# Kernel tuning notes

Hardware: AMD Instinct MI355X
Metric: run time of the kernel (lower is better)

The kernel has to match this reference:

```python
import jax, jax.numpy as jnp
import numpy as np

B, S, C, NH = 4, 2048, 1024, 16
HD = C // NH


def setup_inputs() -> dict:
    key = jax.random.key(0)
    ks = jax.random.split(key, 8)
    w = lambda k, shape: (jax.random.normal(k, shape, dtype=jnp.float32) * 0.02)
    return {
        "x": jax.random.normal(ks[0], (B, S, C), dtype=jnp.float32),
        "y": jax.random.normal(ks[1], (B, S, C), dtype=jnp.float32),
        "mask": jnp.zeros((B, S), dtype=bool),  # True = padded key
        "Wq_w": w(ks[2], (C, C)),
        "Wq_b": jnp.zeros((C,), dtype=jnp.float32),
        "Wkv_w": w(ks[3], (2 * C, C)),
        "Wkv_b": jnp.zeros((2 * C,), dtype=jnp.float32),
        "Wo_w": w(ks[4], (C, C)),
        "Wo_b": jnp.zeros((C,), dtype=jnp.float32),
    }


def reference(x, y, mask, Wq_w, Wq_b, Wkv_w, Wkv_b, Wo_w, Wo_b):
    b, s, c = x.shape
    # projections (torch nn.Linear: x @ W.T + b)
    q = (x @ Wq_w.T + Wq_b).reshape(b, s, NH, HD).transpose(0, 2, 1, 3)  # bhsd
    kv = (y @ Wkv_w.T + Wkv_b).reshape(b, s, 2, NH, HD)
    k = kv[:, :, 0].transpose(0, 2, 1, 3)  # bhsd
    v = kv[:, :, 1].transpose(0, 2, 1, 3)  # bhsd
    # scores: [b, h, s_q, s_k]
    attn = jnp.einsum("bhqd,bhkd->bhqk", q, k) / np.sqrt(HD).astype(np.float32)
    causal = jnp.triu(jnp.ones((s, s), dtype=bool), 1)  # True above diagonal
    combined = causal[None, None] | mask[:, None, None, :]
    attn = jnp.where(combined, -jnp.inf, attn)
    attn = jax.nn.softmax(attn, axis=-1)
    out = jnp.einsum("bhqk,bhkd->bhqd", attn, v)
    out = out.transpose(0, 2, 1, 3).reshape(b, s, c)
    return out @ Wo_w.T + Wo_b
```

## Files before the change

kernel.cpp:

```cpp
#include <hip/hip_runtime.h>
#include <stdint.h>

#define B_  4
#define S_  2048
#define C_  1024
#define NH_ 16
#define HD_ 64
#define M_  (B_*S_)
#define NT_ (S_/64)
#define NKT 16

typedef __attribute__((ext_vector_type(8))) short bf16x8;
typedef __attribute__((ext_vector_type(4))) float f32x4;

typedef __attribute__((address_space(1))) const unsigned int gu32;
typedef __attribute__((address_space(3))) unsigned int lu32;

__device__ __forceinline__ void gload16(const void* g, void* l) {
    __builtin_amdgcn_global_load_lds((gu32*)g, (lu32*)l, 16, 0, 0);
}

__device__ __forceinline__ unsigned short f2bf(float f) {
    union { float f; unsigned u; } v; v.f = f;
    unsigned r = v.u + 0x7FFF + ((v.u >> 16) & 1);
    return (unsigned short)(r >> 16);
}

__global__ __launch_bounds__(256)
void cvt_all(const float4* __restrict__ x, const float4* __restrict__ y,
             const float4* __restrict__ wq, const float4* __restrict__ wkv,
             const float4* __restrict__ wo,
             uint4* __restrict__ xb, uint4* __restrict__ yb, uint4* __restrict__ wqb,
             uint4* __restrict__ wkvb, uint4* __restrict__ wob) {
    int i = blockIdx.x * 256 + threadIdx.x;
    const float4* src; uint4* dst; int off;
    if      (i < 1048576) { src = x;   dst = xb;   off = i; }
    else if (i < 2097152) { src = y;   dst = yb;   off = i - 1048576; }
    else if (i < 2228224) { src = wq;  dst = wqb;  off = i - 2097152; }
    else if (i < 2490368) { src = wkv; dst = wkvb; off = i - 2228224; }
    else                  { src = wo;  dst = wob;  off = i - 2490368; }
    float4 a = src[2*off], b = src[2*off+1];
    union { unsigned short s[8]; uint4 v; } u;
    u.s[0]=f2bf(a.x); u.s[1]=f2bf(a.y); u.s[2]=f2bf(a.z); u.s[3]=f2bf(a.w);
    u.s[4]=f2bf(b.x); u.s[5]=f2bf(b.y); u.s[6]=f2bf(b.z); u.s[7]=f2bf(b.w);
    dst[off] = u.v;
}


#define STAGE_A(mi, kb, db) do { \
    gload16(gA + (size_t)(mi)*64*1024 + (kb),           sh + (db)*32768 + (w*8 + (mi)*64)*64); \
    gload16(gA + ((size_t)(mi)*64 + 128)*1024 + (kb),   sh + (db)*32768 + (w*8 + 128 + (mi)*64)*64); \
} while (0)

#define STAGE_B(ni, kb, db) do { \
    gload16(gB + (size_t)(ni)*32*1024 + (kb),           sh + (db)*32768 + 16384 + ((w>>2)*64 + (w&3)*8 + (ni)*32)*64); \
    gload16(gB + ((size_t)(ni)*32 + 128)*1024 + (kb),   sh + (db)*32768 + 16384 + ((w>>2)*64 + (w&3)*8 + (ni)*32 + 128)*64); \
} while (0)

#define READ_A(half) do { \
    _Pragma("unroll") \
    for (int mf = 0; mf < 4; ++mf) { \
        int idx = (wy*128 + (half)*64 + mf*16 + l16)*64 + colb; \
        af[mf][0] = *(const bf16x8*)&Asb[idx]; \
        af[mf][1] = *(const bf16x8*)&Asb[idx ^ 32]; \
    } \
} while (0)

#define READ_B(half) do { \
    _Pragma("unroll") \
    for (int nf = 0; nf < 2; ++nf) { \
        int idx = (wx*64 + (half)*32 + nf*16 + l16)*64 + colb; \
        bfv[half][nf][0] = *(const bf16x8*)&Bsb[idx]; \
        bfv[half][nf][1] = *(const bf16x8*)&Bsb[idx ^ 32]; \
    } \
} while (0)

#define MFMA_Q(mi, ni) do { \
    _Pragma("unroll") \
    for (int mf = 0; mf < 4; ++mf) { \
        _Pragma("unroll") \
        for (int nf = 0; nf < 2; ++nf) { \
            acc[mi][ni][mf][nf] = __builtin_amdgcn_mfma_f32_16x16x32_bf16(af[mf][0], bfv[ni][nf][0], acc[mi][ni][mf][nf], 0, 0, 0); \
            acc[mi][ni][mf][nf] = __builtin_amdgcn_mfma_f32_16x16x32_bf16(af[mf][1], bfv[ni][nf][1], acc[mi][ni][mf][nf], 0, 0, 0); \
        } \
    } \
} while (0)

template<int MODE>
__device__ __forceinline__
void gemm256_body(const unsigned short* __restrict__ A, const unsigned short* __restrict__ Bt,
                  const float* __restrict__ bias,
                  unsigned short* __restrict__ out0, unsigned short* __restrict__ out1,
                  float* __restrict__ outf, int bx, int by, unsigned short* sh)
{
    const int t = threadIdx.x;
    const int lane = t & 63, w = t >> 6;
    const int quad = lane >> 4, l16 = lane & 15;
    const int wy = w >> 2, wx = w & 3;
    const int s7 = l16 & 7;
    const int colb = (quad ^ s7) << 3;
    const int c16 = (lane & 7) ^ (lane >> 3);

    const int rowA0 = by * 256;
    const int colB0 = bx * 256;

    const unsigned short* gA = A  + (size_t)(rowA0 + w*8 + (lane>>3))*1024 + c16*8;
    const unsigned short* gB = Bt + (size_t)(colB0 + (w>>2)*64 + (w&3)*8 + (lane>>3))*1024 + c16*8;

    f32x4 acc[2][2][4][2] = {};
    bf16x8 af[4][2], bfv[2][2][2];

    STAGE_A(0, 0, 0);
    STAGE_B(1, 0, 0);
    STAGE_B(0, 0, 0);
    STAGE_A(1, 0, 0);
    STAGE_A(0, 64, 1);
    STAGE_B(1, 64, 1);
    asm volatile("s_waitcnt vmcnt(6)" ::: "memory");
    __builtin_amdgcn_s_barrier();
    __builtin_amdgcn_sched_barrier(0);

    #pragma unroll 1
    for (int kt = 0; kt < NKT; ++kt) {
        const int cur = kt & 1;
        const unsigned short* Asb = sh + cur*32768;
        const unsigned short* Bsb = Asb + 16384;
        const int kb1 = (kt + 1) * 64;
        const int kb2 = (kt + 2) * 64;
        const bool st1 = (kt + 1 < NKT);
        const bool st2 = (kt + 2 < NKT);

        if (st1) STAGE_B(0, kb1, cur ^ 1);
        READ_A(0);
        READ_B(0);
        __builtin_amdgcn_s_setprio(1);
        MFMA_Q(0, 0);
        __builtin_amdgcn_s_setprio(0);

        if (st1) STAGE_A(1, kb1, cur ^ 1);
        READ_B(1);
        __builtin_amdgcn_s_setprio(1);
        MFMA_Q(0, 1);
        __builtin_amdgcn_s_setprio(0);
        if (st1) asm volatile("s_waitcnt vmcnt(8)" ::: "memory");
        else     asm volatile("s_waitcnt vmcnt(0)" ::: "memory");
        __builtin_amdgcn_s_barrier();
        __builtin_amdgcn_sched_barrier(0);

        if (st2) STAGE_A(0, kb2, cur);
        READ_A(1);
        __builtin_amdgcn_s_setprio(1);
        MFMA_Q(1, 1);
        __builtin_amdgcn_s_setprio(0);

        if (st2) STAGE_B(1, kb2, cur);
        __builtin_amdgcn_s_setprio(1);
        MFMA_Q(1, 0);
        __builtin_amdgcn_s_setprio(0);
        if      (st2) asm volatile("s_waitcnt vmcnt(6)" ::: "memory");
        else if (st1) asm volatile("s_waitcnt vmcnt(2)" ::: "memory");
        __builtin_amdgcn_s_barrier();
        __builtin_amdgcn_sched_barrier(0);
    }

    const float QSCALE = 0.180336880111f;
    #pragma unroll
    for (int mi = 0; mi < 2; ++mi)
    #pragma unroll
    for (int ni = 0; ni < 2; ++ni)
    #pragma unroll
    for (int nf = 0; nf < 2; ++nf) {
        int gn = colB0 + wx*64 + ni*32 + nf*16 + l16;
        float bv = bias[gn];
        #pragma unroll
        for (int mf = 0; mf < 4; ++mf) {
            #pragma unroll
            for (int r = 0; r < 4; ++r) {
                int gm = rowA0 + wy*128 + mi*64 + mf*16 + quad*4 + r;
                float v = acc[mi][ni][mf][nf][r] + bv;
                if (MODE == 2) {
                    outf[(size_t)gm * 1024 + gn] = v;
                } else if (MODE == 0) {
                    v *= QSCALE;
                    int b = gm >> 11, s = gm & 2047;
                    int h = gn >> 6,  d = gn & 63;
                    out0[(((size_t)(b*NH_ + h)*S_ + s) << 6) + d] = f2bf(v);
                } else {
                    int b = gm >> 11, s = gm & 2047;
                    if (gn < C_) {
                        int h = gn >> 6, d = gn & 63;
                        out0[(((size_t)(b*NH_ + h)*S_ + s) << 6) + d] = f2bf(v);
                    } else {
                        int n2 = gn - C_;
                        int h = n2 >> 6, d = n2 & 63;
                        out1[((size_t)(b*NH_ + h)*HD_ + d)*S_ + s] = f2bf(v);
                    }
                }
            }
        }
    }
}

__global__ __launch_bounds__(512, 2)
void proj_fused256(const unsigned short* __restrict__ xb, const unsigned short* __restrict__ Wqb,
                   const float* __restrict__ Wq_b,
                   const unsigned short* __restrict__ yb, const unsigned short* __restrict__ Wkvb,
                   const float* __restrict__ Wkv_b,
                   unsigned short* __restrict__ Qg, unsigned short* __restrict__ Kg,
                   unsigned short* __restrict__ Vt)
{
    extern __shared__ unsigned short sh[];
    int bid = blockIdx.x;
    int id = (bid & 7) * 48 + (bid >> 3);
    if (id < 128) {
        gemm256_body<0>(xb, Wqb, Wq_b, Qg, nullptr, nullptr, id & 3, id >> 2, sh);
    } else {
        int j = id - 128;
        gemm256_body<1>(yb, Wkvb, Wkv_b, Kg, Vt, nullptr, j & 7, j >> 3, sh);
    }
}

__global__ __launch_bounds__(512, 2)
void gemm_oproj256(const unsigned short* __restrict__ A, const unsigned short* __restrict__ Bt,
                   const float* __restrict__ bias, float* __restrict__ outf)
{
    extern __shared__ unsigned short sh[];
    int id = ((blockIdx.x & 7) << 4) + (blockIdx.x >> 3);
    gemm256_body<2>(A, Bt, bias, nullptr, nullptr, outf, id & 3, id >> 2, sh);
}

__global__ __launch_bounds__(256, 4)
void attn_kernel(const unsigned short* __restrict__ Qg, const unsigned short* __restrict__ Kg,
                 const unsigned short* __restrict__ Vt, const unsigned char* __restrict__ maskp,
                 unsigned short* __restrict__ att)
{
    __shared__ unsigned short Pl[64*72];
    __shared__ float Lbuf[4][64];
    __shared__ float Linv[64];
    int t = threadIdx.x, lane = t & 63, w = t >> 6;
    int quad = lane >> 4, l16 = lane & 15;
    int bh = blockIdx.x, b = bh >> 4, h = bh & 15;
    int qi = blockIdx.y;

    const unsigned short* kbase = Kg + ((size_t)bh*S_ + w*16 + l16)*HD_ + quad*8;
    const unsigned short* vbase = Vt + ((size_t)bh*HD_ + w*16 + l16)*S_ + quad*8;
    int kp_row = w*16 + quad*4;
    const unsigned char* mbase = maskp + (size_t)b*S_ + kp_row;

    for (int half = 0; half < 2; ++half) {
        int qt = half ? (NT_ - 1 - qi) : qi;

        bf16x8 qf[4][2];
        #pragma unroll
        for (int m = 0; m < 4; ++m) {
            const unsigned short* qp = Qg + ((size_t)bh*S_ + qt*64 + m*16 + l16)*HD_;
            qf[m][0] = *reinterpret_cast<const bf16x8*>(qp + quad*8);
            qf[m][1] = *reinterpret_cast<const bf16x8*>(qp + 32 + quad*8);
        }
        f32x4 oacc[4] = {};
        float lsum[4] = {0.f, 0.f, 0.f, 0.f};

        bf16x8 kc0 = *reinterpret_cast<const bf16x8*>(kbase);
        bf16x8 kc1 = *reinterpret_cast<const bf16x8*>(kbase + 32);

        for (int kt = 0; kt <= qt; ++kt) {
            int ktn = (kt < qt) ? kt + 1 : kt;
            const unsigned short* kpn = kbase + (size_t)ktn*64*HD_;
            bf16x8 kn0 = *reinterpret_cast<const bf16x8*>(kpn);
            bf16x8 kn1 = *reinterpret_cast<const bf16x8*>(kpn + 32);
            const unsigned short* vp = vbase + kt*64;
            bf16x8 vc0 = *reinterpret_cast<const bf16x8*>(vp);
            bf16x8 vc1 = *reinterpret_cast<const bf16x8*>(vp + 32);

            unsigned m4 = *reinterpret_cast<const unsigned*>(mbase + kt*64);

            f32x4 sacc[4];
            #pragma unroll
            for (int m = 0; m < 4; ++m) {
                sacc[m] = __builtin_amdgcn_mfma_f32_16x16x32_bf16(kc0, qf[m][0], f32x4{}, 0, 0, 0);
                sacc[m] = __builtin_amdgcn_mfma_f32_16x16x32_bf16(kc1, qf[m][1], sacc[m], 0, 0, 0);
            }

            bool diag = (kt == qt);
            #pragma unroll
            for (int m = 0; m < 4; ++m) {
                float p[4];
                if (diag) {
                    #pragma unroll
                    for (int r = 0; r < 4; ++r) {
                        float s = sacc[m][r];
                        if (kp_row + r > m*16 + l16) s = -1e30f;
                        p[r] = __builtin_amdgcn_exp2f(s);
                    }
                } else {
                    #pragma unroll
                    for (int r = 0; r < 4; ++r)
                        p[r] = __builtin_amdgcn_exp2f(sacc[m][r]);
                }
                if (m4) {
                    #pragma unroll
                    for (int r = 0; r < 4; ++r)
                        if ((m4 >> (8*r)) & 0xFFu) p[r] = 0.f;
                }
                lsum[m] += (p[0] + p[1]) + (p[2] + p[3]);
                unsigned a01 = __builtin_amdgcn_perm(__float_as_uint(p[1]), __float_as_uint(p[0]), 0x07060302u);
                unsigned a23 = __builtin_amdgcn_perm(__float_as_uint(p[3]), __float_as_uint(p[2]), 0x07060302u);
                *reinterpret_cast<uint2*>(&Pl[(m*16 + l16)*72 + w*16 + quad*4]) = make_uint2(a01, a23);
            }
            __syncthreads();
            #pragma unroll
            for (int m = 0; m < 4; ++m) {
                bf16x8 pf0 = *reinterpret_cast<const bf16x8*>(&Pl[(m*16 + l16)*72 + quad*8]);
                bf16x8 pf1 = *reinterpret_cast<const bf16x8*>(&Pl[(m*16 + l16)*72 + 32 + quad*8]);
                oacc[m] = __builtin_amdgcn_mfma_f32_16x16x32_bf16(pf0, vc0, oacc[m], 0, 0, 0);
                oacc[m] = __builtin_amdgcn_mfma_f32_16x16x32_bf16(pf1, vc1, oacc[m], 0, 0, 0);
            }
            __syncthreads();
            kc0 = kn0; kc1 = kn1;
        }

        #pragma unroll
        for (int m = 0; m < 4; ++m) {
            lsum[m] += __shfl_xor(lsum[m], 16, 64);
            lsum[m] += __shfl_xor(lsum[m], 32, 64);
            Lbuf[w][m*16 + l16] = lsum[m];
        }
        __syncthreads();
        int q64 = t & 63;
        Linv[q64] = 1.0f / (Lbuf[0][q64] + Lbuf[1][q64] + Lbuf[2][q64] + Lbuf[3][q64]);
        __syncthreads();
        #pragma unroll
        for (int m = 0; m < 4; ++m) {
            #pragma unroll
            for (int r = 0; r < 4; ++r) {
                float iv = Linv[m*16 + quad*4 + r];
                int q = qt*64 + m*16 + quad*4 + r;
                att[((size_t)(b*S_ + q))*C_ + h*HD_ + w*16 + l16] = f2bf(oacc[m][r] * iv);
            }
        }
        __syncthreads();
    }
}

extern "C" void kernel_launch(void* const* d_in, const int* in_sizes, int n_in,
                              void* d_out, int out_size, void* d_ws, size_t ws_size,
                              hipStream_t stream) {
    const float* x     = (const float*)d_in[0];
    const float* y     = (const float*)d_in[1];
    const unsigned char* mask = (const unsigned char*)d_in[2];
    const float* Wq_w  = (const float*)d_in[3];
    const float* Wq_b  = (const float*)d_in[4];
    const float* Wkv_w = (const float*)d_in[5];
    const float* Wkv_b = (const float*)d_in[6];
    const float* Wo_w  = (const float*)d_in[7];
    const float* Wo_b  = (const float*)d_in[8];
    float* out = (float*)d_out;

    unsigned short* xb   = (unsigned short*)d_ws;
    unsigned short* yb   = xb   + (size_t)M_*C_;
    unsigned short* Wqb  = yb   + (size_t)M_*C_;
    unsigned short* Wkvb = Wqb  + (size_t)C_*C_;
    unsigned short* Wob  = Wkvb + (size_t)2*C_*C_;
    unsigned short* Qg   = Wob  + (size_t)C_*C_;
    unsigned short* Kg   = Qg   + (size_t)M_*C_;
    unsigned short* Vtg  = Kg   + (size_t)M_*C_;
    unsigned short* att  = xb;

    static bool once = []() {
        hipFuncSetAttribute((const void*)proj_fused256, hipFuncAttributeMaxDynamicSharedMemorySize, 131072);
        hipFuncSetAttribute((const void*)gemm_oproj256, hipFuncAttributeMaxDynamicSharedMemorySize, 131072);
        return true;
    }();
    (void)once;

    cvt_all<<<10240, 256, 0, stream>>>((const float4*)x, (const float4*)y,
        (const float4*)Wq_w, (const float4*)Wkv_w, (const float4*)Wo_w,
        (uint4*)xb, (uint4*)yb, (uint4*)Wqb, (uint4*)Wkvb, (uint4*)Wob);

    proj_fused256<<<384, 512, 131072, stream>>>(xb, Wqb, Wq_b, yb, Wkvb, Wkv_b, Qg, Kg, Vtg);
    attn_kernel<<<dim3(B_*NH_, NT_/2), 256, 0, stream>>>(Qg, Kg, Vtg, mask, att);
    gemm_oproj256<<<128, 512, 131072, stream>>>(att, Wob, Wo_b, out);
}
```

Baseline: 322.5 us.

## Shrink GEMM tiles to 256x128 with simpler single-stage prefetch schedule

```diff
diff --git a/kernel.cpp b/kernel.cpp
--- a/kernel.cpp
+++ b/kernel.cpp
@@ -47,43 +47,31 @@
 }
 
 
-#define STAGE_A(mi, kb, db) do { \
-    gload16(gA + (size_t)(mi)*64*1024 + (kb),           sh + (db)*32768 + (w*8 + (mi)*64)*64); \
-    gload16(gA + ((size_t)(mi)*64 + 128)*1024 + (kb),   sh + (db)*32768 + (w*8 + 128 + (mi)*64)*64); \
+#define STAGE_U(u, kb, db) \
+    gload16(gA + (size_t)(u)*64*1024 + (kb), sh + (db)*24576 + ((u)*64 + w*8)*64)
+#define STAGE_V(v, kb, db) \
+    gload16(gB + (size_t)(v)*64*1024 + (kb), sh + (db)*24576 + 16384 + ((v)*64 + w*8)*64)
+#define STAGE_ALL(kb, db) do { \
+    STAGE_U(0, kb, db); STAGE_U(1, kb, db); STAGE_U(2, kb, db); STAGE_U(3, kb, db); \
+    STAGE_V(0, kb, db); STAGE_V(1, kb, db); \
 } while (0)
 
-#define STAGE_B(ni, kb, db) do { \
-    gload16(gB + (size_t)(ni)*32*1024 + (kb),           sh + (db)*32768 + 16384 + ((w>>2)*64 + (w&3)*8 + (ni)*32)*64); \
-    gload16(gB + ((size_t)(ni)*32 + 128)*1024 + (kb),   sh + (db)*32768 + 16384 + ((w>>2)*64 + (w&3)*8 + (ni)*32 + 128)*64); \
+#define READ_AB(h) do { \
+    const int co = colb ^ ((h)*32); \
+    _Pragma("unroll") \
+    for (int mf = 0; mf < 4; ++mf) \
+        af[mf] = *(const bf16x8*)&Asb[(wq*64 + mf*16 + l16)*64 + co]; \
+    _Pragma("unroll") \
+    for (int nf = 0; nf < 4; ++nf) \
+        bfr[nf] = *(const bf16x8*)&Bsb[(wx*64 + nf*16 + l16)*64 + co]; \
 } while (0)
 
-#define READ_A(half) do { \
+#define MFMA16() do { \
     _Pragma("unroll") \
-    for (int mf = 0; mf < 4; ++mf) { \
-        int idx = (wy*128 + (half)*64 + mf*16 + l16)*64 + colb; \
-        af[mf][0] = *(const bf16x8*)&Asb[idx]; \
-        af[mf][1] = *(const bf16x8*)&Asb[idx ^ 32]; \
-    } \
-} while (0)
-
-#define READ_B(half) do { \
-    _Pragma("unroll") \
-    for (int nf = 0; nf < 2; ++nf) { \
-        int idx = (wx*64 + (half)*32 + nf*16 + l16)*64 + colb; \
-        bfv[half][nf][0] = *(const bf16x8*)&Bsb[idx]; \
-        bfv[half][nf][1] = *(const bf16x8*)&Bsb[idx ^ 32]; \
-    } \
-} while (0)
-
-#define MFMA_Q(mi, ni) do { \
-    _Pragma("unroll") \
-    for (int mf = 0; mf < 4; ++mf) { \
+    for (int mf = 0; mf < 4; ++mf) \
         _Pragma("unroll") \
-        for (int nf = 0; nf < 2; ++nf) { \
-            acc[mi][ni][mf][nf] = __builtin_amdgcn_mfma_f32_16x16x32_bf16(af[mf][0], bfv[ni][nf][0], acc[mi][ni][mf][nf], 0, 0, 0); \
-            acc[mi][ni][mf][nf] = __builtin_amdgcn_mfma_f32_16x16x32_bf16(af[mf][1], bfv[ni][nf][1], acc[mi][ni][mf][nf], 0, 0, 0); \
-        } \
-    } \
+        for (int nf = 0; nf < 4; ++nf) \
+            acc[mf][nf] = __builtin_amdgcn_mfma_f32_16x16x32_bf16(af[mf], bfr[nf], acc[mf][nf], 0, 0, 0); \
 } while (0)
 
 template<int MODE>
@@ -96,26 +84,22 @@
     const int t = threadIdx.x;
     const int lane = t & 63, w = t >> 6;
     const int quad = lane >> 4, l16 = lane & 15;
-    const int wy = w >> 2, wx = w & 3;
+    const int wq = w >> 1, wx = w & 1;
     const int s7 = l16 & 7;
     const int colb = (quad ^ s7) << 3;
     const int c16 = (lane & 7) ^ (lane >> 3);
 
     const int rowA0 = by * 256;
-    const int colB0 = bx * 256;
+    const int colB0 = bx * 128;
 
     const unsigned short* gA = A  + (size_t)(rowA0 + w*8 + (lane>>3))*1024 + c16*8;
-    const unsigned short* gB = Bt + (size_t)(colB0 + (w>>2)*64 + (w&3)*8 + (lane>>3))*1024 + c16*8;
-
-    f32x4 acc[2][2][4][2] = {};
-    bf16x8 af[4][2], bfv[2][2][2];
-
-    STAGE_A(0, 0, 0);
-    STAGE_B(1, 0, 0);
-    STAGE_B(0, 0, 0);
-    STAGE_A(1, 0, 0);
-    STAGE_A(0, 64, 1);
-    STAGE_B(1, 64, 1);
+    const unsigned short* gB = Bt + (size_t)(colB0 + w*8 + (lane>>3))*1024 + c16*8;
+
+    f32x4 acc[4][4] = {};
+    bf16x8 af[4], bfr[4];
+
+    STAGE_ALL(0, 0);
+    STAGE_ALL(64, 1);
     asm volatile("s_waitcnt vmcnt(6)" ::: "memory");
     __builtin_amdgcn_s_barrier();
     __builtin_amdgcn_sched_barrier(0);
@@ -123,61 +107,46 @@
     #pragma unroll 1
     for (int kt = 0; kt < NKT; ++kt) {
         const int cur = kt & 1;
-        const unsigned short* Asb = sh + cur*32768;
+        const unsigned short* Asb = sh + cur*24576;
         const unsigned short* Bsb = Asb + 16384;
-        const int kb1 = (kt + 1) * 64;
         const int kb2 = (kt + 2) * 64;
-        const bool st1 = (kt + 1 < NKT);
         const bool st2 = (kt + 2 < NKT);
 
-        if (st1) STAGE_B(0, kb1, cur ^ 1);
-        READ_A(0);
-        READ_B(0);
+        READ_AB(0);
         __builtin_amdgcn_s_setprio(1);
-        MFMA_Q(0, 0);
+        MFMA16();
         __builtin_amdgcn_s_setprio(0);
 
-        if (st1) STAGE_A(1, kb1, cur ^ 1);
-        READ_B(1);
+        READ_AB(1);
+        if (st2) {
+            asm volatile("s_waitcnt lgkmcnt(0)" ::: "memory");
+            __builtin_amdgcn_sched_barrier(0);
+            __builtin_amdgcn_s_barrier();
+            STAGE_ALL(kb2, cur);
+        }
         __builtin_amdgcn_s_setprio(1);
-        MFMA_Q(0, 1);
+        MFMA16();
         __builtin_amdgcn_s_setprio(0);
-        if (st1) asm volatile("s_waitcnt vmcnt(8)" ::: "memory");
-        else     asm volatile("s_waitcnt vmcnt(0)" ::: "memory");
-        __builtin_amdgcn_s_barrier();
-        __builtin_amdgcn_sched_barrier(0);
-
-        if (st2) STAGE_A(0, kb2, cur);
-        READ_A(1);
-        __builtin_amdgcn_s_setprio(1);
-        MFMA_Q(1, 1);
-        __builtin_amdgcn_s_setprio(0);
-
-        if (st2) STAGE_B(1, kb2, cur);
-        __builtin_amdgcn_s_setprio(1);
-        MFMA_Q(1, 0);
-        __builtin_amdgcn_s_setprio(0);
-        if      (st2) asm volatile("s_waitcnt vmcnt(6)" ::: "memory");
-        else if (st1) asm volatile("s_waitcnt vmcnt(2)" ::: "memory");
-        __builtin_amdgcn_s_barrier();
-        __builtin_amdgcn_sched_barrier(0);
+
+        if      (st2)           asm volatile("s_waitcnt vmcnt(6)" ::: "memory");
+        else if (kt == NKT - 2) asm volatile("s_waitcnt vmcnt(0)" ::: "memory");
+        if (kt < NKT - 1) {
+            __builtin_amdgcn_s_barrier();
+            __builtin_amdgcn_sched_barrier(0);
+        }
     }
 
     const float QSCALE = 0.180336880111f;
     #pragma unroll
-    for (int mi = 0; mi < 2; ++mi)
-    #pragma unroll
-    for (int ni = 0; ni < 2; ++ni)
-    #pragma unroll
-    for (int nf = 0; nf < 2; ++nf) {
-        int gn = colB0 + wx*64 + ni*32 + nf*16 + l16;
+    for (int nf = 0; nf < 4; ++nf) {
+        int gn = colB0 + wx*64 + nf*16 + l16;
         float bv = bias[gn];
         #pragma unroll
         for (int mf = 0; mf < 4; ++mf) {
             #pragma unroll
             for (int r = 0; r < 4; ++r) {
-                int gm = rowA0 + wy*128 + mi*64 + mf*16 + quad*4 + r;
-                float v = acc[mi][ni][mf][nf][r] + bv;
+                int gm = rowA0 + wq*64 + mf*16 + quad*4 + r;
+                float v = acc[mf][nf][r] + bv;
                 if (MODE == 2) {
                     outf[(size_t)gm * 1024 + gn] = v;
                 } else if (MODE == 0) {
@@ -211,12 +180,12 @@
 {
     extern __shared__ unsigned short sh[];
     int bid = blockIdx.x;
-    int id = (bid & 7) * 48 + (bid >> 3);
-    if (id < 128) {
-        gemm256_body<0>(xb, Wqb, Wq_b, Qg, nullptr, nullptr, id & 3, id >> 2, sh);
+    int id = (bid & 7) * 96 + (bid >> 3);
+    if (id < 256) {
+        gemm256_body<0>(xb, Wqb, Wq_b, Qg, nullptr, nullptr, id & 7, id >> 3, sh);
     } else {
-        int j = id - 128;
-        gemm256_body<1>(yb, Wkvb, Wkv_b, Kg, Vt, nullptr, j & 7, j >> 3, sh);
+        int j = id - 256;
+        gemm256_body<1>(yb, Wkvb, Wkv_b, Kg, Vt, nullptr, j & 15, j >> 4, sh);
     }
 }
 
@@ -225,8 +194,8 @@
                    const float* __restrict__ bias, float* __restrict__ outf)
 {
     extern __shared__ unsigned short sh[];
-    int id = ((blockIdx.x & 7) << 4) + (blockIdx.x >> 3);
-    gemm256_body<2>(A, Bt, bias, nullptr, nullptr, outf, id & 3, id >> 2, sh);
+    int id = ((blockIdx.x & 7) << 5) + (blockIdx.x >> 3);
+    gemm256_body<2>(A, Bt, bias, nullptr, nullptr, outf, id & 7, id >> 3, sh);
 }
 
 __global__ __launch_bounds__(256, 4)
@@ -367,8 +336,8 @@
     unsigned short* att  = xb;
 
     static bool once = []() {
-        hipFuncSetAttribute((const void*)proj_fused256, hipFuncAttributeMaxDynamicSharedMemorySize, 131072);
-        hipFuncSetAttribute((const void*)gemm_oproj256, hipFuncAttributeMaxDynamicSharedMemorySize, 131072);
+        hipFuncSetAttribute((const void*)proj_fused256, hipFuncAttributeMaxDynamicSharedMemorySize, 98304);
+        hipFuncSetAttribute((const void*)gemm_oproj256, hipFuncAttributeMaxDynamicSharedMemorySize, 98304);
         return true;
     }();
     (void)once;
@@ -377,7 +346,7 @@
         (const float4*)Wq_w, (const float4*)Wkv_w, (const float4*)Wo_w,
         (uint4*)xb, (uint4*)yb, (uint4*)Wqb, (uint4*)Wkvb, (uint4*)Wob);
 
-    proj_fused256<<<384, 512, 131072, stream>>>(xb, Wqb, Wq_b, yb, Wkvb, Wkv_b, Qg, Kg, Vtg);
+    proj_fused256<<<768, 512, 98304, stream>>>(xb, Wqb, Wq_b, yb, Wkvb, Wkv_b, Qg, Kg, Vtg);
     attn_kernel<<<dim3(B_*NH_, NT_/2), 256, 0, stream>>>(Qg, Kg, Vtg, mask, att);
-    gemm_oproj256<<<128, 512, 131072, stream>>>(att, Wob, Wo_b, out);
-}
+    gemm_oproj256<<<256, 512, 98304, stream>>>(att, Wob, Wo_b, out);
+}
```

After: 308.7 us. 1.04x faster.

## Restructure GEMM main loop into barrier-separated ping-pong phases

Applied to the files above, without the earlier changes.

```diff
diff --git a/kernel.cpp b/kernel.cpp
--- a/kernel.cpp
+++ b/kernel.cpp
@@ -57,21 +57,21 @@
     gload16(gB + ((size_t)(ni)*32 + 128)*1024 + (kb),   sh + (db)*32768 + 16384 + ((w>>2)*64 + (w&3)*8 + (ni)*32 + 128)*64); \
 } while (0)
 
-#define READ_A(half) do { \
+#define READ_A(mi) do { \
     _Pragma("unroll") \
     for (int mf = 0; mf < 4; ++mf) { \
-        int idx = (wy*128 + (half)*64 + mf*16 + l16)*64 + colb; \
+        int idx = (wy*128 + (mi)*64 + mf*16 + l16)*64 + colb; \
         af[mf][0] = *(const bf16x8*)&Asb[idx]; \
         af[mf][1] = *(const bf16x8*)&Asb[idx ^ 32]; \
     } \
 } while (0)
 
-#define READ_B(half) do { \
+#define READ_B(ni) do { \
     _Pragma("unroll") \
     for (int nf = 0; nf < 2; ++nf) { \
-        int idx = (wx*64 + (half)*32 + nf*16 + l16)*64 + colb; \
-        bfv[half][nf][0] = *(const bf16x8*)&Bsb[idx]; \
-        bfv[half][nf][1] = *(const bf16x8*)&Bsb[idx ^ 32]; \
+        int idx = (wx*64 + (ni)*32 + nf*16 + l16)*64 + colb; \
+        bfv[ni][nf][0] = *(const bf16x8*)&Bsb[idx]; \
+        bfv[ni][nf][1] = *(const bf16x8*)&Bsb[idx ^ 32]; \
     } \
 } while (0)
 
@@ -84,6 +84,18 @@
             acc[mi][ni][mf][nf] = __builtin_amdgcn_mfma_f32_16x16x32_bf16(af[mf][1], bfv[ni][nf][1], acc[mi][ni][mf][nf], 0, 0, 0); \
         } \
     } \
+} while (0)
+
+#define PHASE_MID() do { \
+    __builtin_amdgcn_s_barrier(); \
+    asm volatile("s_waitcnt lgkmcnt(0)" ::: "memory"); \
+    __builtin_amdgcn_sched_barrier(0); \
+    __builtin_amdgcn_s_setprio(1); \
+} while (0)
+
+#define PHASE_END() do { \
+    __builtin_amdgcn_s_barrier(); \
+    __builtin_amdgcn_sched_barrier(0); \
 } while (0)
 
 template<int MODE>
@@ -130,37 +142,40 @@
         const bool st1 = (kt + 1 < NKT);
         const bool st2 = (kt + 2 < NKT);
 
-        if (st1) STAGE_B(0, kb1, cur ^ 1);
         READ_A(0);
         READ_B(0);
-        __builtin_amdgcn_s_setprio(1);
+        if (st1) STAGE_B(0, kb1, cur ^ 1);
+        asm volatile("s_waitcnt lgkmcnt(8)" ::: "memory");
+        PHASE_MID();
         MFMA_Q(0, 0);
         __builtin_amdgcn_s_setprio(0);
-
+        PHASE_END();
+
+        READ_B(1);
         if (st1) STAGE_A(1, kb1, cur ^ 1);
-        READ_B(1);
-        __builtin_amdgcn_s_setprio(1);
+        PHASE_MID();
         MFMA_Q(0, 1);
         __builtin_amdgcn_s_setprio(0);
         if (st1) asm volatile("s_waitcnt vmcnt(8)" ::: "memory");
         else     asm volatile("s_waitcnt vmcnt(0)" ::: "memory");
+        PHASE_END();
+
+        READ_A(1);
+        if (st2) STAGE_A(0, kb2, cur);
+        PHASE_MID();
+        MFMA_Q(1, 1);
+        __builtin_amdgcn_s_setprio(0);
+        PHASE_END();
+
+        if (st2) STAGE_B(1, kb2, cur);
         __builtin_amdgcn_s_barrier();
         __builtin_amdgcn_sched_barrier(0);
-
-        if (st2) STAGE_A(0, kb2, cur);
-        READ_A(1);
-        __builtin_amdgcn_s_setprio(1);
-        MFMA_Q(1, 1);
-        __builtin_amdgcn_s_setprio(0);
-
-        if (st2) STAGE_B(1, kb2, cur);
         __builtin_amdgcn_s_setprio(1);
         MFMA_Q(1, 0);
         __builtin_amdgcn_s_setprio(0);
         if      (st2) asm volatile("s_waitcnt vmcnt(6)" ::: "memory");
         else if (st1) asm volatile("s_waitcnt vmcnt(2)" ::: "memory");
-        __builtin_amdgcn_s_barrier();
-        __builtin_amdgcn_sched_barrier(0);
+        PHASE_END();
     }
 
     const float QSCALE = 0.180336880111f;
```

Result: no change. 326.4 us (+1.2%).
